# Optimization experiments

Hardware: AMD Instinct MI355X
Metric: run time of the kernel (lower is better)

## Reference

```python
import jax, jax.numpy as jnp
import numpy as np

B, T, I, H = 4096, 512, 3, 50


def setup_inputs() -> dict:
    key = jax.random.key(0)
    ks = jax.random.split(key, 11)
    s_i, s_h = 1.0 / np.sqrt(H), 1.0 / np.sqrt(H)
    return {
        "x": jax.random.normal(ks[0], (B, T, I), jnp.float32),
        "W_ih0": jax.random.normal(ks[1], (4 * H, I), jnp.float32) * s_i,
        "W_hh0": jax.random.normal(ks[2], (4 * H, H), jnp.float32) * s_h,
        "b_ih0": jax.random.normal(ks[3], (4 * H,), jnp.float32) * s_h,
        "b_hh0": jax.random.normal(ks[4], (4 * H,), jnp.float32) * s_h,
        "W_ih1": jax.random.normal(ks[5], (4 * H, H), jnp.float32) * s_h,
        "W_hh1": jax.random.normal(ks[6], (4 * H, H), jnp.float32) * s_h,
        "b_ih1": jax.random.normal(ks[7], (4 * H,), jnp.float32) * s_h,
        "b_hh1": jax.random.normal(ks[8], (4 * H,), jnp.float32) * s_h,
        "W_fc": jax.random.normal(ks[9], (1, H), jnp.float32) * s_h,
        "b_fc": jax.random.normal(ks[10], (1,), jnp.float32) * s_h,
    }


def _lstm_layer(x, W_ih, W_hh, b_ih, b_hh):
    # x: [B, T, D_in] -> hidden sequence [B, T, H]. PyTorch gate order i|f|g|o.
    Bt, H_ = x.shape[0], W_hh.shape[1]
    # Precompute input contribution for all timesteps (one big GEMM).
    xg = jnp.einsum('btd,gd->btg', x, W_ih) + (b_ih + b_hh)  # [B, T, 4H]

    def step(carry, xg_t):
        h, c = carry
        g = xg_t + h @ W_hh.T  # [B, 4H]
        i, f, gg, o = jnp.split(g, 4, axis=-1)
        i, f, o = jax.nn.sigmoid(i), jax.nn.sigmoid(f), jax.nn.sigmoid(o)
        c = f * c + i * jnp.tanh(gg)
        h = o * jnp.tanh(c)
        return (h, c), h

    h0 = jnp.zeros((Bt, H_), x.dtype)
    c0 = jnp.zeros((Bt, H_), x.dtype)
    (_, _), hs = jax.lax.scan(step, (h0, c0), xg.transpose(1, 0, 2))  # hs: [T, B, H]
    return hs.transpose(1, 0, 2)


def reference(x, W_ih0, W_hh0, b_ih0, b_hh0, W_ih1, W_hh1, b_ih1, b_hh1, W_fc, b_fc):
    # 2-layer LSTM, zero initial state; dropout between layers is inactive (eval mode).
    h1 = _lstm_layer(x, W_ih0, W_hh0, b_ih0, b_hh0)
    h2 = _lstm_layer(h1, W_ih1, W_hh1, b_ih1, b_hh1)
    return h2[:, -1, :] @ W_fc.T + b_fc  # [B, 1]
```

## Files before the change

kernel.cpp:

```cpp
#include <hip/hip_runtime.h>

#define SEQT 512
#define BM   16
#define NW   7
#define NT   (NW * 64)
#define ROWB 256
#define HBUF 4096

typedef _Float16 half8  __attribute__((ext_vector_type(8)));
typedef _Float16 half4v __attribute__((ext_vector_type(4)));
typedef float    f32x4  __attribute__((ext_vector_type(4)));

__device__ __forceinline__ float fast_rcp(float x) { return __builtin_amdgcn_rcpf(x); }
__device__ __forceinline__ float sigm(float x) { return fast_rcp(1.f + __expf(-x)); }
__device__ __forceinline__ float tanh_f(float x) { return 1.f - 2.f * fast_rcp(__expf(2.f * x) + 1.f); }

#define MFMA16(A, B, C) __builtin_amdgcn_mfma_f32_16x16x32_f16((A), (B), (C), 0, 0, 0)


__global__ __launch_bounds__(NT) void lstm2_mfma5(
    const float* __restrict__ x,
    const float* __restrict__ Wih0, const float* __restrict__ Whh0,
    const float* __restrict__ bih0, const float* __restrict__ bhh0,
    const float* __restrict__ Wih1, const float* __restrict__ Whh1,
    const float* __restrict__ bih1, const float* __restrict__ bhh1,
    const float* __restrict__ Wfc,  const float* __restrict__ bfc,
    float* __restrict__ out)
{
    __shared__ __align__(16) char hb[2 * HBUF];
    __shared__ float fcbuf[NW][BM];

    const int tid = threadIdx.x;
    const int l   = tid & 63, w = tid >> 6;
    const int m   = l & 15,  g4 = l >> 4;
    const int b0  = blockIdx.x * BM;
    const int swz = (m & 7) << 4;
    const bool hasT1 = (w < 6);

    half8 a0[2][2];
    half8 a1[2][4];
    float wfcv[2];
    int   ucv[2];
    bool  wok[2];
#pragma unroll
    for (int tt = 0; tt < 2; ++tt) {
        const int T  = 2 * w + tt;
        const int nA = T * 16 + m;
        const int uA = nA >> 2, gA = nA & 3;
        const bool ok = uA < 50;
        const int rA = gA * 50 + (ok ? uA : 0);
#pragma unroll
        for (int kt = 0; kt < 2; ++kt) {
            half8 v;
#pragma unroll
            for (int j = 0; j < 8; ++j) {
                const int k = kt * 32 + g4 * 8 + j;
                float f = 0.f;
                if (ok) {
                    if (k < 50)                 f = Whh0[rA * 50 + k];
                    else if (k >= 52 && k < 55) f = Wih0[rA * 3 + (k - 52)];
                    else if (k == 55)           f = bih0[rA] + bhh0[rA];
                }
                v[j] = (_Float16)f;
            }
            a0[tt][kt] = v;
        }
#pragma unroll
        for (int kt = 0; kt < 4; ++kt) {
            half8 v;
#pragma unroll
            for (int j = 0; j < 8; ++j) {
                const int k = kt * 32 + g4 * 8 + j;
                float f = 0.f;
                if (ok) {
                    if (k < 50)                  f = Wih1[rA * 50 + k];
                    else if (k == 55)            f = bih1[rA] + bhh1[rA];
                    else if (k >= 64 && k < 114) f = Whh1[rA * 50 + (k - 64)];
                }
                v[j] = (_Float16)f;
            }
            a1[tt][kt] = v;
        }
        const int uc = T * 4 + g4;
        ucv[tt]  = uc;
        wok[tt]  = (uc < 50);
        wfcv[tt] = (uc < 50) ? Wfc[uc] : 0.f;
    }

    int rd[4], wr0[2], wr1[2];
#pragma unroll
    for (int q = 0; q < 4; ++q) rd[q] = m * ROWB + (((q * 4 + g4) * 16) ^ swz);
#pragma unroll
    for (int tt = 0; tt < 2; ++tt) {
        wr0[tt] = m * ROWB + ((ucv[tt] * 2) ^ swz);
        wr1[tt] = m * ROWB + (((64 + ucv[tt]) * 2) ^ swz);
    }
    const int wrx = m * ROWB + (104 ^ swz);

    for (int i = tid; i < 2 * HBUF / 4; i += NT) ((int*)hb)[i] = 0;
    __syncthreads();
    const bool xlane = (w == 0) && (g4 == 0);
    const float* xbase = x + (size_t)(b0 + m) * (SEQT * 3);
    const _Float16 onef = (_Float16)1.f;
    if (xlane) {
        half4v xv;
        xv[0] = (_Float16)xbase[0]; xv[1] = (_Float16)xbase[1];
        xv[2] = (_Float16)xbase[2]; xv[3] = onef;
        *(half4v*)(hb + HBUF + wrx) = xv;
        half4v z; z[0] = (_Float16)0.f; z[1] = z[0]; z[2] = z[0]; z[3] = onef;
        *(half4v*)(hb + wrx) = z;
    }
    float c0[2] = {0.f, 0.f}, c1[2] = {0.f, 0.f}, h1v[2] = {0.f, 0.f};
    __syncthreads();

    const f32x4 z4 = {0.f, 0.f, 0.f, 0.f};

    auto phase = [&](int rb, int wb, bool doL1, bool doX, int t) {
        const half8 bf0 = *(const half8*)(hb + rb + rd[0]);
        const half8 bf1 = *(const half8*)(hb + rb + rd[1]);
        const half8 bf2 = *(const half8*)(hb + rb + rd[2]);
        const half8 bf3 = *(const half8*)(hb + rb + rd[3]);

        f32x4 gA0, gA1, gB0, gB1;
        gA0 = MFMA16(a0[0][0], bf0, z4); gA0 = MFMA16(a0[0][1], bf1, gA0);
        if (hasT1) { gA1 = MFMA16(a0[1][0], bf0, z4); gA1 = MFMA16(a0[1][1], bf1, gA1); }
        if (doL1) {
            f32x4 p = MFMA16(a1[0][0], bf0, z4); p = MFMA16(a1[0][1], bf1, p);
            f32x4 q = MFMA16(a1[0][2], bf2, z4); q = MFMA16(a1[0][3], bf3, q);
            gB0 = p + q;
            if (hasT1) {
                f32x4 r = MFMA16(a1[1][0], bf0, z4); r = MFMA16(a1[1][1], bf1, r);
                f32x4 s = MFMA16(a1[1][2], bf2, z4); s = MFMA16(a1[1][3], bf3, s);
                gB1 = r + s;
            }
        }

#pragma unroll
        for (int tt = 0; tt < 2; ++tt) {
            if (tt == 1 && !hasT1) break;
            const f32x4 g0v = (tt == 0) ? gA0 : gA1;
            const float i0 = sigm(g0v[0]), f0 = sigm(g0v[1]);
            const float gg0 = tanh_f(g0v[2]), o0 = sigm(g0v[3]);
            c0[tt] = f0 * c0[tt] + i0 * gg0;
            const float h0 = o0 * tanh_f(c0[tt]);
            if (wok[tt]) *(_Float16*)(hb + wb + wr0[tt]) = (_Float16)h0;
            if (doL1) {
                const f32x4 g1v = (tt == 0) ? gB0 : gB1;
                const float i1 = sigm(g1v[0]), f1 = sigm(g1v[1]);
                const float gg1 = tanh_f(g1v[2]), o1 = sigm(g1v[3]);
                c1[tt] = f1 * c1[tt] + i1 * gg1;
                h1v[tt] = o1 * tanh_f(c1[tt]);
                if (wok[tt]) *(_Float16*)(hb + wb + wr1[tt]) = (_Float16)h1v[tt];
            }
        }
        if (doX && xlane) {
            const float* xp = xbase + (t + 1) * 3;
            half4v xv;
            xv[0] = (_Float16)xp[0]; xv[1] = (_Float16)xp[1];
            xv[2] = (_Float16)xp[2]; xv[3] = onef;
            *(half4v*)(hb + wb + wrx) = xv;
        }
        __syncthreads();
    };

    phase(HBUF, 0, false, true, 0);
    for (int it = 0; it < 255; ++it) {
        phase(0, HBUF, true, true, 2 * it + 1);
        phase(HBUF, 0, true, true, 2 * it + 2);
    }
    phase(0, HBUF, true, false, 511);

    {
        const half8 bf0 = *(const half8*)(hb + HBUF + rd[0]);
        const half8 bf1 = *(const half8*)(hb + HBUF + rd[1]);
        const half8 bf2 = *(const half8*)(hb + HBUF + rd[2]);
        const half8 bf3 = *(const half8*)(hb + HBUF + rd[3]);
#pragma unroll
        for (int tt = 0; tt < 2; ++tt) {
            if (tt == 1 && !hasT1) break;
            f32x4 p = MFMA16(a1[tt][0], bf0, z4); p = MFMA16(a1[tt][1], bf1, p);
            f32x4 q = MFMA16(a1[tt][2], bf2, z4); q = MFMA16(a1[tt][3], bf3, q);
            const f32x4 g1v = p + q;
            const float i1 = sigm(g1v[0]), f1 = sigm(g1v[1]);
            const float gg1 = tanh_f(g1v[2]), o1 = sigm(g1v[3]);
            c1[tt] = f1 * c1[tt] + i1 * gg1;
            h1v[tt] = o1 * tanh_f(c1[tt]);
        }
    }

    float pv = h1v[0] * wfcv[0] + h1v[1] * wfcv[1];
    pv += __shfl_down(pv, 32, 64);
    pv += __shfl_down(pv, 16, 64);
    if (l < 16) fcbuf[w][l] = pv;
    __syncthreads();
    if (tid < BM) {
        float s = bfc[0];
#pragma unroll
        for (int ww = 0; ww < NW; ++ww) s += fcbuf[ww][tid];
        out[b0 + tid] = s;
    }
}

extern "C" void kernel_launch(void* const* d_in, const int* in_sizes, int n_in,
                              void* d_out, int out_size, void* d_ws, size_t ws_size,
                              hipStream_t stream)
{
    const float* x    = (const float*)d_in[0];
    const float* Wih0 = (const float*)d_in[1];
    const float* Whh0 = (const float*)d_in[2];
    const float* bih0 = (const float*)d_in[3];
    const float* bhh0 = (const float*)d_in[4];
    const float* Wih1 = (const float*)d_in[5];
    const float* Whh1 = (const float*)d_in[6];
    const float* bih1 = (const float*)d_in[7];
    const float* bhh1 = (const float*)d_in[8];
    const float* Wfc  = (const float*)d_in[9];
    const float* bfc  = (const float*)d_in[10];
    float* out = (float*)d_out;

    const int B = in_sizes[0] / (SEQT * 3);
    lstm2_mfma5<<<B / BM, NT, 0, stream>>>(x, Wih0, Whh0, bih0, bhh0,
                                           Wih1, Whh1, bih1, bhh1, Wfc, bfc, out);
}
```

Baseline: 540.1 us.

## Redistribute LSTM tiles across four waves and share reciprocals in gate math

Shrinks the block from seven waves to four and spreads the 26 gate tiles (13 per layer) round-robin across those waves, so each wave handles up to seven tiles and a 64-slot MFMA weight array in registers. The gate activations now share reciprocals: one rcp covers the i and f sigmoids and one covers g and o. The x input is prefetched one step ahead into a register, and the final FC projection gathers h through shared memory instead of a shuffle reduction. The aim is to cut barrier and wave-count overhead per timestep and reduce transcendental work, at the cost of more serial MFMA and VALU work per wave and heavy register pressure.

```diff
diff --git a/kernel.cpp b/kernel.cpp
--- a/kernel.cpp
+++ b/kernel.cpp
@@ -2,23 +2,68 @@
 
 #define SEQT 512
 #define BM   16
-#define NW   7
+#define NW   4
 #define NT   (NW * 64)
 #define ROWB 256
 #define HBUF 4096
+#define NUNITS 26
 
 typedef _Float16 half8  __attribute__((ext_vector_type(8)));
 typedef _Float16 half4v __attribute__((ext_vector_type(4)));
 typedef float    f32x4  __attribute__((ext_vector_type(4)));
 
 __device__ __forceinline__ float fast_rcp(float x) { return __builtin_amdgcn_rcpf(x); }
-__device__ __forceinline__ float sigm(float x) { return fast_rcp(1.f + __expf(-x)); }
-__device__ __forceinline__ float tanh_f(float x) { return 1.f - 2.f * fast_rcp(__expf(2.f * x) + 1.f); }
 
 #define MFMA16(A, B, C) __builtin_amdgcn_mfma_f32_16x16x32_f16((A), (B), (C), 0, 0, 0)
 
 
-__global__ __launch_bounds__(NT) void lstm2_mfma5(
+template<int CW>
+__device__ __forceinline__ void phase_body(
+    int t, const half8* bf, half8 (&af)[7][4], float (&cst)[7],
+    char* hbase, int wb, const int (&wrh)[7], const bool (&wok)[7], float (&h1v)[7])
+{
+    constexpr int NU = (CW < 2) ? 7 : 6;
+    const f32x4 z4 = {0.f, 0.f, 0.f, 0.f};
+    f32x4 g[7];
+#pragma unroll
+    for (int idx = 0; idx < NU; ++idx) {
+        constexpr int U_BASE = CW;
+        const int unit = U_BASE + 4 * idx;
+        if (unit < 13) {
+            f32x4 a = MFMA16(af[idx][0], bf[0], z4);
+            g[idx]  = MFMA16(af[idx][1], bf[1], a);
+        } else {
+            f32x4 p = MFMA16(af[idx][0], bf[0], z4);
+            p       = MFMA16(af[idx][1], bf[1], p);
+            f32x4 q = MFMA16(af[idx][2], bf[2], z4);
+            q       = MFMA16(af[idx][3], bf[3], q);
+            g[idx]  = p + q;
+        }
+    }
+#pragma unroll
+    for (int idx = 0; idx < NU; ++idx) {
+        const int unit = CW + 4 * idx;
+        const bool isL1 = (unit >= 13);
+        if (isL1 && t == 0) continue;
+        const f32x4 gv = g[idx];
+        const float Ei = __expf(-gv[0]), Ef = __expf(-gv[1]);
+        const float Eg = __expf(2.f * gv[2]), Eo = __expf(-gv[3]);
+        const float pi = 1.f + Ei, pf = 1.f + Ef, pg = 1.f + Eg, po = 1.f + Eo;
+        const float r1 = fast_rcp(pi * pf);
+        const float iv = pf * r1, fv = pi * r1;
+        const float r2 = fast_rcp(pg * po);
+        const float ov = pg * r2;
+        const float tg = 1.f - 2.f * (po * r2);
+        const float c  = fv * cst[idx] + iv * tg;
+        cst[idx] = c;
+        const float Ec = __expf(2.f * c);
+        const float hv = ov * (1.f - 2.f * fast_rcp(1.f + Ec));
+        if (isL1) h1v[idx] = hv;
+        if (wok[idx]) *(_Float16*)(hbase + wb + wrh[idx]) = (_Float16)hv;
+    }
+}
+
+__global__ __launch_bounds__(NT) void lstm2_mfma7(
     const float* __restrict__ x,
     const float* __restrict__ Wih0, const float* __restrict__ Whh0,
     const float* __restrict__ bih0, const float* __restrict__ bhh0,
@@ -28,80 +73,69 @@
     float* __restrict__ out)
 {
     __shared__ __align__(16) char hb[2 * HBUF];
-    __shared__ float fcbuf[NW][BM];
+    __shared__ float h1g[52][BM];
 
     const int tid = threadIdx.x;
     const int l   = tid & 63, w = tid >> 6;
     const int m   = l & 15,  g4 = l >> 4;
     const int b0  = blockIdx.x * BM;
     const int swz = (m & 7) << 4;
-    const bool hasT1 = (w < 6);
-
-    half8 a0[2][2];
-    half8 a1[2][4];
-    float wfcv[2];
-    int   ucv[2];
-    bool  wok[2];
-#pragma unroll
-    for (int tt = 0; tt < 2; ++tt) {
-        const int T  = 2 * w + tt;
-        const int nA = T * 16 + m;
+
+    half8 af[7][4];
+    float cst[7], h1v[7];
+    int   wrh[7], ucA[7];
+    bool  wok[7];
+#pragma unroll
+    for (int idx = 0; idx < 7; ++idx) {
+        cst[idx] = 0.f; h1v[idx] = 0.f; wrh[idx] = 0; ucA[idx] = 0; wok[idx] = false;
+        const int unit = w + 4 * idx;
+        if (unit >= NUNITS) continue;
+        const int layer = unit / 13, tile = unit % 13;
+        const int nA = tile * 16 + m;
         const int uA = nA >> 2, gA = nA & 3;
         const bool ok = uA < 50;
         const int rA = gA * 50 + (ok ? uA : 0);
-#pragma unroll
-        for (int kt = 0; kt < 2; ++kt) {
+        const int nkt = (layer == 0) ? 2 : 4;
+#pragma unroll
+        for (int kt = 0; kt < 4; ++kt) {
+            if (kt >= nkt) continue;
             half8 v;
 #pragma unroll
             for (int j = 0; j < 8; ++j) {
                 const int k = kt * 32 + g4 * 8 + j;
                 float f = 0.f;
                 if (ok) {
-                    if (k < 50)                 f = Whh0[rA * 50 + k];
-                    else if (k >= 52 && k < 55) f = Wih0[rA * 3 + (k - 52)];
-                    else if (k == 55)           f = bih0[rA] + bhh0[rA];
+                    if (layer == 0) {
+                        if (k < 50)                 f = Whh0[rA * 50 + k];
+                        else if (k >= 52 && k < 55) f = Wih0[rA * 3 + (k - 52)];
+                        else if (k == 55)           f = bih0[rA] + bhh0[rA];
+                    } else {
+                        if (k < 50)                  f = Wih1[rA * 50 + k];
+                        else if (k == 55)            f = bih1[rA] + bhh1[rA];
+                        else if (k >= 64 && k < 114) f = Whh1[rA * 50 + (k - 64)];
+                    }
                 }
                 v[j] = (_Float16)f;
             }
-            a0[tt][kt] = v;
-        }
-#pragma unroll
-        for (int kt = 0; kt < 4; ++kt) {
-            half8 v;
-#pragma unroll
-            for (int j = 0; j < 8; ++j) {
-                const int k = kt * 32 + g4 * 8 + j;
-                float f = 0.f;
-                if (ok) {
-                    if (k < 50)                  f = Wih1[rA * 50 + k];
-                    else if (k == 55)            f = bih1[rA] + bhh1[rA];
-                    else if (k >= 64 && k < 114) f = Whh1[rA * 50 + (k - 64)];
-                }
-                v[j] = (_Float16)f;
-            }
-            a1[tt][kt] = v;
-        }
-        const int uc = T * 4 + g4;
-        ucv[tt]  = uc;
-        wok[tt]  = (uc < 50);
-        wfcv[tt] = (uc < 50) ? Wfc[uc] : 0.f;
-    }
-
-    int rd[4], wr0[2], wr1[2];
+            af[idx][kt] = v;
+        }
+        const int uc = tile * 4 + g4;
+        ucA[idx] = uc;
+        wok[idx] = (uc < 50);
+        wrh[idx] = m * ROWB + ((((layer == 0 ? 0 : 64) + uc) * 2) ^ swz);
+    }
+
+    int rd[4];
 #pragma unroll
     for (int q = 0; q < 4; ++q) rd[q] = m * ROWB + (((q * 4 + g4) * 16) ^ swz);
-#pragma unroll
-    for (int tt = 0; tt < 2; ++tt) {
-        wr0[tt] = m * ROWB + ((ucv[tt] * 2) ^ swz);
-        wr1[tt] = m * ROWB + (((64 + ucv[tt]) * 2) ^ swz);
-    }
     const int wrx = m * ROWB + (104 ^ swz);
 
     for (int i = tid; i < 2 * HBUF / 4; i += NT) ((int*)hb)[i] = 0;
     __syncthreads();
-    const bool xlane = (w == 0) && (g4 == 0);
+    const bool xlane = (w == 3) && (g4 == 0);
     const float* xbase = x + (size_t)(b0 + m) * (SEQT * 3);
     const _Float16 onef = (_Float16)1.f;
+    half4v xpk;
     if (xlane) {
         half4v xv;
         xv[0] = (_Float16)xbase[0]; xv[1] = (_Float16)xbase[1];
@@ -109,94 +143,67 @@
         *(half4v*)(hb + HBUF + wrx) = xv;
         half4v z; z[0] = (_Float16)0.f; z[1] = z[0]; z[2] = z[0]; z[3] = onef;
         *(half4v*)(hb + wrx) = z;
-    }
-    float c0[2] = {0.f, 0.f}, c1[2] = {0.f, 0.f}, h1v[2] = {0.f, 0.f};
+        xpk[0] = (_Float16)xbase[3]; xpk[1] = (_Float16)xbase[4];
+        xpk[2] = (_Float16)xbase[5]; xpk[3] = onef;
+    }
     __syncthreads();
 
-    const f32x4 z4 = {0.f, 0.f, 0.f, 0.f};
-
-    auto phase = [&](int rb, int wb, bool doL1, bool doX, int t) {
-        const half8 bf0 = *(const half8*)(hb + rb + rd[0]);
-        const half8 bf1 = *(const half8*)(hb + rb + rd[1]);
-        const half8 bf2 = *(const half8*)(hb + rb + rd[2]);
-        const half8 bf3 = *(const half8*)(hb + rb + rd[3]);
-
-        f32x4 gA0, gA1, gB0, gB1;
-        gA0 = MFMA16(a0[0][0], bf0, z4); gA0 = MFMA16(a0[0][1], bf1, gA0);
-        if (hasT1) { gA1 = MFMA16(a0[1][0], bf0, z4); gA1 = MFMA16(a0[1][1], bf1, gA1); }
-        if (doL1) {
-            f32x4 p = MFMA16(a1[0][0], bf0, z4); p = MFMA16(a1[0][1], bf1, p);
-            f32x4 q = MFMA16(a1[0][2], bf2, z4); q = MFMA16(a1[0][3], bf3, q);
-            gB0 = p + q;
-            if (hasT1) {
-                f32x4 r = MFMA16(a1[1][0], bf0, z4); r = MFMA16(a1[1][1], bf1, r);
-                f32x4 s = MFMA16(a1[1][2], bf2, z4); s = MFMA16(a1[1][3], bf3, s);
-                gB1 = r + s;
+    for (int t = 0; t < SEQT; ++t) {
+        const int rb = ((t + 1) & 1) * HBUF;
+        const int wb = (t & 1) * HBUF;
+        half8 bf[4];
+#pragma unroll
+        for (int q = 0; q < 4; ++q) bf[q] = *(const half8*)(hb + rb + rd[q]);
+
+        if      (w == 0) phase_body<0>(t, bf, af, cst, hb, wb, wrh, wok, h1v);
+        else if (w == 1) phase_body<1>(t, bf, af, cst, hb, wb, wrh, wok, h1v);
+        else if (w == 2) phase_body<2>(t, bf, af, cst, hb, wb, wrh, wok, h1v);
+        else             phase_body<3>(t, bf, af, cst, hb, wb, wrh, wok, h1v);
+
+        if (xlane) {
+            if (t < SEQT - 1) *(half4v*)(hb + wb + wrx) = xpk;
+            if (t < SEQT - 2) {
+                const float* xp = xbase + (t + 2) * 3;
+                xpk[0] = (_Float16)xp[0]; xpk[1] = (_Float16)xp[1];
+                xpk[2] = (_Float16)xp[2]; xpk[3] = onef;
             }
         }
-
-#pragma unroll
-        for (int tt = 0; tt < 2; ++tt) {
-            if (tt == 1 && !hasT1) break;
-            const f32x4 g0v = (tt == 0) ? gA0 : gA1;
-            const float i0 = sigm(g0v[0]), f0 = sigm(g0v[1]);
-            const float gg0 = tanh_f(g0v[2]), o0 = sigm(g0v[3]);
-            c0[tt] = f0 * c0[tt] + i0 * gg0;
-            const float h0 = o0 * tanh_f(c0[tt]);
-            if (wok[tt]) *(_Float16*)(hb + wb + wr0[tt]) = (_Float16)h0;
-            if (doL1) {
-                const f32x4 g1v = (tt == 0) ? gB0 : gB1;
-                const float i1 = sigm(g1v[0]), f1 = sigm(g1v[1]);
-                const float gg1 = tanh_f(g1v[2]), o1 = sigm(g1v[3]);
-                c1[tt] = f1 * c1[tt] + i1 * gg1;
-                h1v[tt] = o1 * tanh_f(c1[tt]);
-                if (wok[tt]) *(_Float16*)(hb + wb + wr1[tt]) = (_Float16)h1v[tt];
-            }
-        }
-        if (doX && xlane) {
-            const float* xp = xbase + (t + 1) * 3;
-            half4v xv;
-            xv[0] = (_Float16)xp[0]; xv[1] = (_Float16)xp[1];
-            xv[2] = (_Float16)xp[2]; xv[3] = onef;
-            *(half4v*)(hb + wb + wrx) = xv;
-        }
         __syncthreads();
-    };
-
-    phase(HBUF, 0, false, true, 0);
-    for (int it = 0; it < 255; ++it) {
-        phase(0, HBUF, true, true, 2 * it + 1);
-        phase(HBUF, 0, true, true, 2 * it + 2);
-    }
-    phase(0, HBUF, true, false, 511);
+    }
 
     {
-        const half8 bf0 = *(const half8*)(hb + HBUF + rd[0]);
-        const half8 bf1 = *(const half8*)(hb + HBUF + rd[1]);
-        const half8 bf2 = *(const half8*)(hb + HBUF + rd[2]);
-        const half8 bf3 = *(const half8*)(hb + HBUF + rd[3]);
-#pragma unroll
-        for (int tt = 0; tt < 2; ++tt) {
-            if (tt == 1 && !hasT1) break;
-            f32x4 p = MFMA16(a1[tt][0], bf0, z4); p = MFMA16(a1[tt][1], bf1, p);
-            f32x4 q = MFMA16(a1[tt][2], bf2, z4); q = MFMA16(a1[tt][3], bf3, q);
-            const f32x4 g1v = p + q;
-            const float i1 = sigm(g1v[0]), f1 = sigm(g1v[1]);
-            const float gg1 = tanh_f(g1v[2]), o1 = sigm(g1v[3]);
-            c1[tt] = f1 * c1[tt] + i1 * gg1;
-            h1v[tt] = o1 * tanh_f(c1[tt]);
-        }
-    }
-
-    float pv = h1v[0] * wfcv[0] + h1v[1] * wfcv[1];
-    pv += __shfl_down(pv, 32, 64);
-    pv += __shfl_down(pv, 16, 64);
-    if (l < 16) fcbuf[w][l] = pv;
+        half8 bf[4];
+#pragma unroll
+        for (int q = 0; q < 4; ++q) bf[q] = *(const half8*)(hb + HBUF + rd[q]);
+        const f32x4 z4 = {0.f, 0.f, 0.f, 0.f};
+#pragma unroll
+        for (int idx = 0; idx < 7; ++idx) {
+            const int unit = w + 4 * idx;
+            if (unit < 13 || unit >= NUNITS) continue;
+            f32x4 p = MFMA16(af[idx][0], bf[0], z4);
+            p       = MFMA16(af[idx][1], bf[1], p);
+            f32x4 q = MFMA16(af[idx][2], bf[2], z4);
+            q       = MFMA16(af[idx][3], bf[3], q);
+            const f32x4 gv = p + q;
+            const float Ei = __expf(-gv[0]), Ef = __expf(-gv[1]);
+            const float Eg = __expf(2.f * gv[2]), Eo = __expf(-gv[3]);
+            const float pi = 1.f + Ei, pf = 1.f + Ef, pg = 1.f + Eg, po = 1.f + Eo;
+            const float r1 = fast_rcp(pi * pf);
+            const float iv = pf * r1, fv = pi * r1;
+            const float r2 = fast_rcp(pg * po);
+            const float ov = pg * r2;
+            const float tg = 1.f - 2.f * (po * r2);
+            const float c  = fv * cst[idx] + iv * tg;
+            const float Ec = __expf(2.f * c);
+            const float hv = ov * (1.f - 2.f * fast_rcp(1.f + Ec));
+            if (wok[idx]) h1g[ucA[idx]][m] = hv;
+        }
+    }
     __syncthreads();
+
     if (tid < BM) {
         float s = bfc[0];
-#pragma unroll
-        for (int ww = 0; ww < NW; ++ww) s += fcbuf[ww][tid];
+        for (int u = 0; u < 50; ++u) s += h1g[u][tid] * Wfc[u];
         out[b0 + tid] = s;
     }
 }
@@ -219,6 +226,6 @@
     float* out = (float*)d_out;
 
     const int B = in_sizes[0] / (SEQT * 3);
-    lstm2_mfma5<<<B / BM, NT, 0, stream>>>(x, Wih0, Whh0, bih0, bhh0,
+    lstm2_mfma7<<<B / BM, NT, 0, stream>>>(x, Wih0, Whh0, bih0, bhh0,
                                            Wih1, Whh1, bih1, bhh1, Wfc, bfc, out);
 }
```

Result: slower. 632.1 us (+17.0%).
